# Kernel tuning notes

Hardware: AMD Instinct MI355X
Metric: run time of the kernel (lower is better)

Reference implementation:

```python
import jax, jax.numpy as jnp
import numpy as np
import math

K = 7
PAD = 3

def _aniso_kernel(k, sigma_h, sigma_v, angle):
    ax = np.linspace(-(k // 2), k // 2, k, dtype=np.float32)
    xx, yy = np.meshgrid(ax, ax, indexing='ij')
    x_rot = xx * math.cos(angle) + yy * math.sin(angle)
    y_rot = -xx * math.sin(angle) + yy * math.cos(angle)
    ker = np.exp(-(x_rot ** 2 / (2 * sigma_h ** 2) + y_rot ** 2 / (2 * sigma_v ** 2)))
    ker = ker / (ker.sum() + 1e-8)
    return jnp.asarray(ker, dtype=jnp.float32)  # (k,k)

BASE_H = _aniso_kernel(K, 2.5, 1.0, 0.0)
BASE_V = _aniso_kernel(K, 2.5, 1.0, math.pi / 2)

def setup_inputs() -> dict:
    key = jax.random.key(0)
    k1, k2, k3, k4 = jax.random.split(key, 4)
    B, C, H, W, MID = 8, 256, 128, 128, 16
    x = jax.random.normal(k1, (B, C, H, W), dtype=jnp.float32)
    angle_map = jax.random.uniform(k2, (B, H, W), dtype=jnp.float32) * math.pi
    w_reduce = jax.random.normal(k3, (MID, C), dtype=jnp.float32) * 0.05
    w_expand = jax.random.normal(k4, (C, MID), dtype=jnp.float32) * 0.05
    return {"x": x, "angle_map": angle_map, "w_reduce": w_reduce, "w_expand": w_expand}

def reference(x, angle_map, w_reduce, w_expand):
    B, C, H, W = x.shape
    # 1x1 conv reduce: (B,C,H,W) x (mid,C) -> (B,mid,H,W)
    x_low = jnp.einsum('bchw,mc->bmhw', x, w_reduce)
    # per-pixel blend weights
    w_h = jnp.cos(angle_map) ** 2                      # (B,H,W)
    combined = (w_h[..., None, None] * BASE_H
                + (1.0 - w_h)[..., None, None] * BASE_V)  # (B,H,W,k,k)
    combined = combined.reshape(B, H, W, K * K)
    # reflect pad and extract kxk patches (stride 1 -> output spatial == H,W)
    x_pad = jnp.pad(x_low, ((0, 0), (0, 0), (PAD, PAD), (PAD, PAD)), mode='reflect')
    patches = jnp.stack(
        [x_pad[:, :, i:i + H, j:j + W] for i in range(K) for j in range(K)],
        axis=-1)                                       # (B,mid,H,W,k*k)
    out_low = jnp.einsum('bmhwk,bhwk->bmhw', patches, combined)
    out_low = jnp.nan_to_num(out_low)
    out = jnp.einsum('bmhw,cm->bchw', out_low, w_expand)
    return jnp.nan_to_num(out)
```

## Files before the change

### kernel.cpp

```cpp
#include <hip/hip_runtime.h>

#define Bn   8
#define Cn   256
#define MIDn 16
#define Hn   128
#define Wn   128
#define HWn  (Hn * Wn)

__global__ __launch_bounds__(256, 4) void reduce_k(const float2* __restrict__ x2,
                                                   const float* __restrict__ wr,
                                                   float2* __restrict__ xlow2) {
    __shared__ float2 comb[4][MIDn][64];

    const int tid = threadIdx.x;
    const int p2  = tid & 63;
    const int wv  = tid >> 6;
    const int b   = blockIdx.y;
    const int p0  = blockIdx.x * 64;

    const int c0 = __builtin_amdgcn_readfirstlane(wv << 6);

    const float2* xb = x2 + ((size_t)b * Cn + c0) * (HWn / 2) + p0 + p2;

    float2 acc[MIDn];
#pragma unroll
    for (int m = 0; m < MIDn; ++m) acc[m] = make_float2(0.f, 0.f);

#pragma unroll 8
    for (int c = 0; c < 64; ++c) {
        const float2 v = xb[(size_t)c * (HWn / 2)];
        const float* w = wr + (c0 + c);
#pragma unroll
        for (int m = 0; m < MIDn; ++m) {
            const float wm = w[m * Cn];
            acc[m].x = fmaf(v.x, wm, acc[m].x);
            acc[m].y = fmaf(v.y, wm, acc[m].y);
        }
    }

#pragma unroll
    for (int m = 0; m < MIDn; ++m) comb[wv][m][p2] = acc[m];
    __syncthreads();

    float2* ob = xlow2 + (size_t)b * MIDn * (HWn / 2) + p0;
#pragma unroll
    for (int k = 0; k < 4; ++k) {
        const int idx = k * 256 + tid;
        const int m   = idx >> 6;
        const int q   = idx & 63;
        const float2 s0 = comb[0][m][q];
        const float2 s1 = comb[1][m][q];
        const float2 s2 = comb[2][m][q];
        const float2 s3 = comb[3][m][q];
        float2 s;
        s.x = (s0.x + s1.x) + (s2.x + s3.x);
        s.y = (s0.y + s1.y) + (s2.y + s3.y);
        ob[(size_t)m * (HWn / 2) + q] = s;
    }
}

#define TW 32
#define TH 4
#define HR (TH + 6)
#define WR (TW + 6)
#define NPX (TH * TW)

__device__ __forceinline__ int reflect_i(int i, int n) {
    return i < 0 ? -i : (i >= n ? 2 * n - 2 - i : i);
}

__global__ __launch_bounds__(256, 4) void conv_expand_k(const float* __restrict__ xlow,
                                                        const float* __restrict__ ang,
                                                        const float* __restrict__ we,
                                                        float2* __restrict__ out2) {
    __shared__ float tile[MIDn][HR][WR];
    __shared__ float low[MIDn][NPX];

    const int tid = threadIdx.x;
    const int b   = blockIdx.y;
    const int rem = blockIdx.x;
    const int th0 = (rem >> 2) * TH;
    const int tw0 = (rem & 3) * TW;

    const float* pb = xlow + (size_t)b * MIDn * HWn;
    for (int idx = tid; idx < MIDn * HR * WR; idx += 256) {
        const int m  = idx / (HR * WR);
        const int r2 = idx - m * (HR * WR);
        const int r  = r2 / WR;
        const int cc = r2 - r * WR;
        const int gr = reflect_i(th0 + r - 3, Hn);
        const int gc = reflect_i(tw0 + cc - 3, Wn);
        tile[m][r][cc] = pb[(size_t)m * HWn + gr * Wn + gc];
    }
    __syncthreads();

    {
        const int px = tid & (NPX - 1);
        const int mh = tid >> 7;
        const int pr = px >> 5;
        const int pc = px & 31;

        const float a  = ang[(size_t)b * HWn + (th0 + pr) * Wn + (tw0 + pc)];
        const float ch = cosf(a);
        const float wh = ch * ch;

        const float fu[7] = {0.48675226f, 0.72614904f, 0.92311635f, 1.0f,
                             0.92311635f, 0.72614904f, 0.48675226f};
        const float fv[7] = {0.011108997f, 0.13533528f, 0.60653066f, 1.0f,
                             0.60653066f, 0.13533528f, 0.011108997f};
        const float su = 1.f + 2.f * (0.48675226f + 0.72614904f + 0.92311635f);
        const float sv = 1.f + 2.f * (0.011108997f + 0.13533528f + 0.60653066f);
        const float inv = 1.f / (su * sv + 1e-8f);
        const float aH = wh * inv;
        const float aV = (1.f - wh) * inv;

        float wcomb[49];
#pragma unroll
        for (int i = 0; i < 7; ++i)
#pragma unroll
            for (int j = 0; j < 7; ++j)
                wcomb[i * 7 + j] = aH * (fu[i] * fv[j]) + aV * (fv[i] * fu[j]);

        const int m0 = mh * 8;
#pragma unroll
        for (int mm = 0; mm < 8; ++mm) {
            float acc = 0.f;
#pragma unroll
            for (int i = 0; i < 7; ++i)
#pragma unroll
                for (int j = 0; j < 7; ++j)
                    acc = fmaf(wcomb[i * 7 + j], tile[m0 + mm][pr + i][pc + j], acc);
            low[m0 + mm][px] = acc;
        }
    }
    __syncthreads();

    const int p2 = tid & 63;
    const int c0 = __builtin_amdgcn_readfirstlane((tid >> 6) << 6);

    const float2* low2 = (const float2*)low;
    float2 lw[MIDn];
#pragma unroll
    for (int m = 0; m < MIDn; ++m) lw[m] = low2[m * 64 + p2];

    const int gh  = th0 + (p2 >> 4);
    const int gw2 = (tw0 >> 1) + (p2 & 15);
    float2* ob = out2 + ((size_t)b * Cn + c0) * (HWn / 2) + gh * (Wn / 2) + gw2;

#pragma unroll 4
    for (int ci = 0; ci < 64; ++ci) {
        const float* w = we + (size_t)(c0 + ci) * MIDn;
        float2 o = make_float2(0.f, 0.f);
#pragma unroll
        for (int m = 0; m < MIDn; ++m) {
            o.x = fmaf(w[m], lw[m].x, o.x);
            o.y = fmaf(w[m], lw[m].y, o.y);
        }
        ob[(size_t)ci * (HWn / 2)] = o;
    }
}

extern "C" void kernel_launch(void* const* d_in, const int* in_sizes, int n_in,
                              void* d_out, int out_size, void* d_ws, size_t ws_size,
                              hipStream_t stream) {
    const float* x   = (const float*)d_in[0];
    const float* ang = (const float*)d_in[1];
    const float* wr  = (const float*)d_in[2];
    const float* we  = (const float*)d_in[3];
    float*       out = (float*)d_out;

    float* xlow = (float*)d_ws;

    reduce_k<<<dim3((HWn / 2) / 64, Bn), dim3(256), 0, stream>>>(
        (const float2*)x, wr, (float2*)xlow);
    conv_expand_k<<<dim3(128, Bn), dim3(256), 0, stream>>>(xlow, ang, we, (float2*)out);
}
```

Measured before the change: 258.8 us.

## Exploit separable Gaussian bases to replace 7x7 blended stencil with two separable passes

The per-pixel 7x7 kernel is a blend of two separable Gaussians, so the convolution is split into a vertical 1D pass over each tile column (computing both the fu and fv filtered rows) and a horizontal 1D pass per output pixel, with symmetric taps paired to halve multiplies. This removes the 49-FMA-per-channel-per-pixel stencil and the 49-entry per-thread weight array. In exchange it adds an extra LDS round trip and two extra barriers, and intermediate results overwrite the tile in place.

```diff
diff --git a/kernel.cpp b/kernel.cpp
--- a/kernel.cpp
+++ b/kernel.cpp
@@ -64,6 +64,7 @@
 #define HR (TH + 6)
 #define WR (TW + 6)
 #define NPX (TH * TW)
+#define NSTRIP (MIDn * WR)
 
 __device__ __forceinline__ int reflect_i(int i, int n) {
     return i < 0 ? -i : (i >= n ? 2 * n - 2 - i : i);
@@ -81,6 +82,15 @@
     const int rem = blockIdx.x;
     const int th0 = (rem >> 2) * TH;
     const int tw0 = (rem & 3) * TW;
+
+    const int px = tid & (NPX - 1);
+    const int mh = tid >> 7;
+    const int pr = px >> 5;
+    const int pc = px & 31;
+    const float a = ang[(size_t)b * HWn + (th0 + pr) * Wn + (tw0 + pc)];
+
+    const float fu0 = 0.48675226f, fu1 = 0.72614904f, fu2 = 0.92311635f;
+    const float fv0 = 0.011108997f, fv1 = 0.13533528f, fv2 = 0.60653066f;
 
     const float* pb = xlow + (size_t)b * MIDn * HWn;
     for (int idx = tid; idx < MIDn * HR * WR; idx += 256) {
@@ -94,43 +104,100 @@
     }
     __syncthreads();
 
+    float oA[8], oB[8], oC[8];
+    int mA, cA, mB, cB, mC, cC;
+    bool hasC;
     {
-        const int px = tid & (NPX - 1);
-        const int mh = tid >> 7;
-        const int pr = px >> 5;
-        const int pc = px & 31;
-
-        const float a  = ang[(size_t)b * HWn + (th0 + pr) * Wn + (tw0 + pc)];
+        {
+            const int s = tid;
+            mA = s / WR; cA = s - mA * WR;
+            float t[HR];
+#pragma unroll
+            for (int r = 0; r < HR; ++r) t[r] = tile[mA][r][cA];
+#pragma unroll
+            for (int r = 0; r < TH; ++r) {
+                const float p06 = t[r] + t[r + 6];
+                const float p15 = t[r + 1] + t[r + 5];
+                const float p24 = t[r + 2] + t[r + 4];
+                const float p3  = t[r + 3];
+                oA[r]     = fmaf(fu0, p06, fmaf(fu1, p15, fmaf(fu2, p24, p3)));
+                oA[4 + r] = fmaf(fv0, p06, fmaf(fv1, p15, fmaf(fv2, p24, p3)));
+            }
+        }
+        {
+            const int s = tid + 256;
+            mB = s / WR; cB = s - mB * WR;
+            float t[HR];
+#pragma unroll
+            for (int r = 0; r < HR; ++r) t[r] = tile[mB][r][cB];
+#pragma unroll
+            for (int r = 0; r < TH; ++r) {
+                const float p06 = t[r] + t[r + 6];
+                const float p15 = t[r + 1] + t[r + 5];
+                const float p24 = t[r + 2] + t[r + 4];
+                const float p3  = t[r + 3];
+                oB[r]     = fmaf(fu0, p06, fmaf(fu1, p15, fmaf(fu2, p24, p3)));
+                oB[4 + r] = fmaf(fv0, p06, fmaf(fv1, p15, fmaf(fv2, p24, p3)));
+            }
+        }
+        hasC = (tid + 512) < NSTRIP;
+        {
+            const int s = hasC ? (tid + 512) : tid;
+            mC = s / WR; cC = s - mC * WR;
+            float t[HR];
+#pragma unroll
+            for (int r = 0; r < HR; ++r) t[r] = tile[mC][r][cC];
+#pragma unroll
+            for (int r = 0; r < TH; ++r) {
+                const float p06 = t[r] + t[r + 6];
+                const float p15 = t[r + 1] + t[r + 5];
+                const float p24 = t[r + 2] + t[r + 4];
+                const float p3  = t[r + 3];
+                oC[r]     = fmaf(fu0, p06, fmaf(fu1, p15, fmaf(fu2, p24, p3)));
+                oC[4 + r] = fmaf(fv0, p06, fmaf(fv1, p15, fmaf(fv2, p24, p3)));
+            }
+        }
+    }
+    __syncthreads();
+
+#pragma unroll
+    for (int r = 0; r < TH; ++r) {
+        tile[mA][r][cA]     = oA[r];
+        tile[mA][4 + r][cA] = oA[4 + r];
+        tile[mB][r][cB]     = oB[r];
+        tile[mB][4 + r][cB] = oB[4 + r];
+    }
+    if (hasC) {
+#pragma unroll
+        for (int r = 0; r < TH; ++r) {
+            tile[mC][r][cC]     = oC[r];
+            tile[mC][4 + r][cC] = oC[4 + r];
+        }
+    }
+    __syncthreads();
+
+    {
         const float ch = cosf(a);
         const float wh = ch * ch;
-
-        const float fu[7] = {0.48675226f, 0.72614904f, 0.92311635f, 1.0f,
-                             0.92311635f, 0.72614904f, 0.48675226f};
-        const float fv[7] = {0.011108997f, 0.13533528f, 0.60653066f, 1.0f,
-                             0.60653066f, 0.13533528f, 0.011108997f};
         const float su = 1.f + 2.f * (0.48675226f + 0.72614904f + 0.92311635f);
         const float sv = 1.f + 2.f * (0.011108997f + 0.13533528f + 0.60653066f);
         const float inv = 1.f / (su * sv + 1e-8f);
         const float aH = wh * inv;
         const float aV = (1.f - wh) * inv;
 
-        float wcomb[49];
-#pragma unroll
-        for (int i = 0; i < 7; ++i)
-#pragma unroll
-            for (int j = 0; j < 7; ++j)
-                wcomb[i * 7 + j] = aH * (fu[i] * fv[j]) + aV * (fv[i] * fu[j]);
-
         const int m0 = mh * 8;
 #pragma unroll
         for (int mm = 0; mm < 8; ++mm) {
-            float acc = 0.f;
-#pragma unroll
-            for (int i = 0; i < 7; ++i)
-#pragma unroll
-                for (int j = 0; j < 7; ++j)
-                    acc = fmaf(wcomb[i * 7 + j], tile[m0 + mm][pr + i][pc + j], acc);
-            low[m0 + mm][px] = acc;
+            const int m = m0 + mm;
+            const float h06 = tile[m][pr][pc] + tile[m][pr][pc + 6];
+            const float h15 = tile[m][pr][pc + 1] + tile[m][pr][pc + 5];
+            const float h24 = tile[m][pr][pc + 2] + tile[m][pr][pc + 4];
+            const float accH = fmaf(fv0, h06, fmaf(fv1, h15, fmaf(fv2, h24, tile[m][pr][pc + 3])));
+            const float g06 = tile[m][4 + pr][pc] + tile[m][4 + pr][pc + 6];
+            const float g15 = tile[m][4 + pr][pc + 1] + tile[m][4 + pr][pc + 5];
+            const float g24 = tile[m][4 + pr][pc + 2] + tile[m][4 + pr][pc + 4];
+            const float accV = fmaf(fu0, g06, fmaf(fu1, g15, fmaf(fu2, g24, tile[m][4 + pr][pc + 3])));
+            low[m][px] = fmaf(aH, accH, aV * accV);
         }
     }
     __syncthreads();
```

Result: no change. 257.9 us (-0.4%).
